# Optimization experiments

Measured on AMD Instinct MI355X. Metric: run time of the kernel, lower is better.

The kernel has to match this reference:

```python
import jax, jax.numpy as jnp
import numpy as np
import math

B, N, D = 128, 64, 2
H, M, L = 64, 64, 2
OMEGA = 1.0


def setup_inputs() -> dict:
    key = jax.random.key(0)
    ks = jax.random.split(key, 32)
    s = 0.1  # param scale
    rn = lambda k, shp: jax.random.normal(k, shp, dtype=jnp.float32) * s
    inp = {
        "x": jax.random.normal(ks[0], (B, N, D), dtype=jnp.float32),
        "spin": jnp.zeros((B, N, 1), jnp.float32),
        "node_w1": rn(ks[1], (D + 1, H)), "node_b1": rn(ks[2], (H,)),
        "node_w2": rn(ks[3], (H, H)), "node_b2": rn(ks[4], (H,)),
        "edge_w1": rn(ks[5], (D + 2, M)), "edge_b1": rn(ks[6], (M,)),
        "edge_w2": rn(ks[7], (M, M)), "edge_b2": rn(ks[8], (M,)),
        "v2e_w1": rn(ks[9], (L, H + M, M)), "v2e_b1": rn(ks[10], (L, M)),
        "v2e_w2": rn(ks[11], (L, M, M)), "v2e_b2": rn(ks[12], (L, M)),
        "e2v_w1": rn(ks[13], (L, M, H)), "e2v_b1": rn(ks[14], (L, H)),
        "e2v_w2": rn(ks[15], (L, H, H)), "e2v_b2": rn(ks[16], (L, H)),
        "head_w1": rn(ks[17], (H, H)), "head_b1": rn(ks[18], (H,)),
        "head_w2": rn(ks[19], (H, D)), "head_b2": rn(ks[20], (D,)),
        # bf_scale_init=0.3 -> softplus-inverse
        "scale": jnp.array([math.log(math.exp(0.3) - 1.0)], jnp.float32),
    }
    return inp


def _mlp(x, w1, b1, w2, b2, act):
    return act(x @ w1 + b1) @ w2 + b2


def reference(x, spin, node_w1, node_b1, node_w2, node_b2,
              edge_w1, edge_b1, edge_w2, edge_b2,
              v2e_w1, v2e_b1, v2e_w2, v2e_b2,
              e2v_w1, e2v_b1, e2v_w2, e2v_b2,
              head_w1, head_b1, head_w2, head_b2, scale):
    gelu = lambda t: jax.nn.gelu(t, approximate=False)  # torch exact GELU
    b, n, d = x.shape
    xs = x * jnp.float32(math.sqrt(OMEGA))
    # node embedding: [B,N,H]
    hv = _mlp(jnp.concatenate([xs, spin], -1), node_w1, node_b1, node_w2, node_b2, gelu)
    # dense pairwise edge features; dr[b,i,j] = xs[b,j] - xs[b,i]
    dr = xs[:, None, :, :] - xs[:, :, None, :]            # [B,N,N,D]
    r2 = jnp.sum(dr * dr, axis=-1, keepdims=True)          # [B,N,N,1]
    rr = jnp.sqrt(r2 + 1e-12)
    he = _mlp(jnp.concatenate([dr, rr, r2], -1), edge_w1, edge_b1, edge_w2, edge_b2, gelu)  # [B,N,N,M]
    # mask excludes self-edges (i==j) from aggregation (they were never created
    # in the original edge list; their dense entries never influence off-diag values)
    mask = (1.0 - jnp.eye(n, dtype=x.dtype))[None, :, :, None]
    inv = jnp.float32(1.0 / max(n - 1, 1))
    for l in range(v2e_w1.shape[0]):
        hvb = jnp.broadcast_to(hv[:, :, None, :], (b, n, n, hv.shape[-1]))  # source node i
        he = _mlp(jnp.concatenate([hvb, he], -1), v2e_w1[l], v2e_b1[l], v2e_w2[l], v2e_b2[l], gelu)
        m = _mlp(he, e2v_w1[l], e2v_b1[l], e2v_w2[l], e2v_b2[l], gelu)      # [B,N,N,H]
        hv = hv + jnp.sum(m * mask, axis=1) * inv           # scatter-add over sources i into j
    dx = _mlp(hv, head_w1, head_b1, head_w2, head_b2, jnp.tanh) * jax.nn.softplus(scale[0])
    return dx - jnp.mean(dx, axis=1, keepdims=True)
```

## Files before the change

kernel.cpp:

```cpp
#include <hip/hip_runtime.h>
#include <math.h>


typedef unsigned short u16;
typedef unsigned int u32;
typedef _Float16 half8 __attribute__((ext_vector_type(8)));
typedef __attribute__((ext_vector_type(4))) float floatx4;

#define TS 72
#define HROW 72
#define HBLK (64 * HROW)

__device__ __forceinline__ float gelu_f(float x) {
    float s = fabsf(x) * 0.70710678118654752f;
    float q = fmaf(fmaf(fmaf(fmaf(0.078108f, s, 0.000972f), s, 0.230389f), s, 0.278393f), s, 1.0f);
    float q2 = q * q;
    float r = __builtin_amdgcn_rcpf(q2 * q2);
    float t = 0.5f * x * r;
    return x > 0.f ? x - t : t;
}

__global__ __launch_bounds__(256) void k_pre(
    const float* __restrict__ ew2, const float* __restrict__ w1he0,
    const float* __restrict__ w2_0, const float* __restrict__ u1_0,
    const float* __restrict__ w1he1, const float* __restrict__ w2_1,
    const float* __restrict__ u1_1,
    const float* __restrict__ eb2, const float* __restrict__ b2_0,
    const float* __restrict__ c1_0, const float* __restrict__ b2_1,
    const float* __restrict__ c1_1,
    const float* __restrict__ b1_0v, const float* __restrict__ b1nv,
    const float* __restrict__ u2_0, const float* __restrict__ u2_1,
    const float* __restrict__ w1n, const float* __restrict__ hw1,
    _Float16* __restrict__ WF,
    float* __restrict__ biasB, float* __restrict__ biasC, float* __restrict__ biasD,
    float* __restrict__ u2_0T, float* __restrict__ u2_1T,
    float* __restrict__ w1nT, float* __restrict__ hw1T,
    const float* __restrict__ x, const float* __restrict__ spin,
    const float* __restrict__ nw1, const float* __restrict__ nb1,
    const float* __restrict__ nw2, const float* __restrict__ nb2,
    const float* __restrict__ w1_0,
    float* __restrict__ hv, float* __restrict__ p0)
{
    int blk = blockIdx.x;
    if (blk < 64) {
        int s = blk >> 4;
        int idx = (blk & 15) * 256 + threadIdx.x;
        int k = idx >> 6, n = idx & 63;
        const float *A, *Bm;
        if (s == 0)      { A = ew2;  Bm = w1he0; }
        else if (s == 1) { A = w2_0; Bm = u1_0;  }
        else if (s == 2) { A = w2_0; Bm = w1he1; }
        else             { A = w2_1; Bm = u1_1;  }
        float acc = 0.f;
        for (int q = 0; q < 64; ++q) acc = fmaf(A[k * 64 + q], Bm[q * 64 + n], acc);
        int kc = k >> 5, qd = (k >> 3) & 3, jj = k & 7;
        WF[(((s * 2 + kc) * 64 + n) * 4 + qd) * 8 + jj] = (_Float16)acc;
    } else if (blk == 64) {
        int s = threadIdx.x >> 6, cc = threadIdx.x & 63;
        if (s > 0) {
            const float *bv, *Bm, *add; float* dst;
            if (s == 1)      { bv = b2_0; Bm = u1_0;  add = c1_0; dst = biasB; }
            else if (s == 2) { bv = b2_0; Bm = w1he1; add = b1nv; dst = biasC; }
            else             { bv = b2_1; Bm = u1_1;  add = c1_1; dst = biasD; }
            float acc = add[cc];
            for (int q = 0; q < 64; ++q) acc = fmaf(bv[q], Bm[q * 64 + cc], acc);
            dst[cc] = acc;
        }
    } else if (blk < 129) {
        int idx = (blk - 65) * 256 + threadIdx.x;
        int s = idx >> 12, r = idx & 4095, m = r >> 6, tc = r & 63;
        const float* W = s == 0 ? u2_0 : s == 1 ? u2_1 : s == 2 ? w1n : hw1;
        float* WT      = s == 0 ? u2_0T : s == 1 ? u2_1T : s == 2 ? w1nT : hw1T;
        WT[tc * 64 + m] = W[m * 64 + tc];
    } else {
        __shared__ float a[4][64];
        __shared__ float shv[4][64];
        int w = threadIdx.x >> 6, h = threadIdx.x & 63;
        int node = (blk - 129) * 4 + w;
        float2 xv = ((const float2*)x)[node];
        float sp = spin[node];
        float z = fmaf(xv.x, nw1[h], fmaf(xv.y, nw1[64 + h], fmaf(sp, nw1[128 + h], nb1[h])));
        a[w][h] = gelu_f(z);
        float acc = nb2[h];
        for (int k = 0; k < 64; ++k) acc = fmaf(a[w][k], nw2[k * 64 + h], acc);
        hv[node * 64 + h] = acc;
        shv[w][h] = acc;
        float pa = b1_0v[h];
        for (int q = 0; q < 64; ++q) pa = fmaf(eb2[q], w1he0[q * 64 + h], pa);
        for (int k = 0; k < 64; ++k) pa = fmaf(shv[w][k], w1_0[k * 64 + h], pa);
        p0[node * 64 + h] = pa;
    }
}

__device__ __forceinline__ void mfma_acc2(
    const _Float16* __restrict__ tA0, const _Float16* __restrict__ tA1,
    const _Float16* __restrict__ WF,
    int stage, int c, int quad, int nn, floatx4 acc0[4], floatx4 acc1[4])
{
    int sA = ((nn >> 2) & 3) << 3;
    #pragma unroll
    for (int kc = 0; kc < 2; ++kc) {
        half8 bf = *(const half8*)(WF + (((stage * 2 + kc) * 64 + c) * 4 + quad) * 8);
        int k0 = (kc * 32 + quad * 8) ^ sA;
        #pragma unroll
        for (int mt = 0; mt < 4; ++mt) {
            half8 af0 = *(const half8*)(tA0 + (mt * 16 + nn) * TS + k0);
            half8 af1 = *(const half8*)(tA1 + (mt * 16 + nn) * TS + k0);
            acc0[mt] = __builtin_amdgcn_mfma_f32_16x16x32_f16(af0, bf, acc0[mt], 0, 0, 0);
            acc1[mt] = __builtin_amdgcn_mfma_f32_16x16x32_f16(af1, bf, acc1[mt], 0, 0, 0);
        }
    }
}

__device__ __forceinline__ void init_bias(floatx4 acc[4], float bc) {
    #pragma unroll
    for (int mt = 0; mt < 4; ++mt) acc[mt] = (floatx4){bc, bc, bc, bc};
}
__device__ __forceinline__ void init_p(floatx4 acc[4], const float* __restrict__ p,
                                       int rowbase, int c, int quad) {
    #pragma unroll
    for (int mt = 0; mt < 4; ++mt)
        #pragma unroll
        for (int r = 0; r < 4; ++r)
            acc[mt][r] = p[(rowbase + mt * 16 + quad * 4 + r) * 64 + c];
}

__global__ __launch_bounds__(256, 4) void k_L0(
    const float* __restrict__ x,
    const float* __restrict__ ew1, const float* __restrict__ eb1,
    const float* __restrict__ p0,
    const float* __restrict__ biasB,
    const float* __restrict__ u2_0T, const float* __restrict__ c2_0,
    const _Float16* __restrict__ WF,
    const float* __restrict__ hv0, float* __restrict__ hv1,
    const float* __restrict__ w1nT, const float* __restrict__ biasC,
    float* __restrict__ p1,
    u16* __restrict__ he0g)
{
    __shared__ __align__(16) _Float16 tA0[64 * TS];
    __shared__ __align__(16) _Float16 tA1[64 * TS];
    __shared__ float sS0[64], sS1[64];
    __shared__ float shv[2][64];
    __shared__ float sredA[256], sredB[256];
    int t = threadIdx.x, L = t & 63;
    int w = __builtin_amdgcn_readfirstlane(t >> 6);
    int nn = L & 15, quad = L >> 4;
    int c = w * 16 + nn;
    int cw = c ^ (quad << 3);
    int b = blockIdx.x >> 5, jp = blockIdx.x & 31;
    int j0 = jp * 2, j1 = j0 + 1;

    float2 xi = ((const float2*)x)[b * 64 + L];
    float2 xa = ((const float2*)x)[b * 64 + j0];
    float2 xb = ((const float2*)x)[b * 64 + j1];
    float da0 = xa.x - xi.x, da1 = xa.y - xi.y;
    float r2a = fmaf(da0, da0, da1 * da1);
    float rra = sqrtf(r2a + 1e-12f);
    float db0 = xb.x - xi.x, db1 = xb.y - xi.y;
    float r2b = fmaf(db0, db0, db1 * db1);
    float rrb = sqrtf(r2b + 1e-12f);
    int swL = ((L >> 2) & 3) << 3;

    #pragma unroll
    for (int mb = 0; mb < 2; ++mb) {
        int m0 = w * 16 + mb * 8;
        half8 h8a, h8b;
        #pragma unroll
        for (int kk = 0; kk < 8; ++kk) {
            int m = m0 + kk;
            float e0 = ew1[m], e1 = ew1[64 + m], e2 = ew1[128 + m], e3 = ew1[192 + m], e4 = eb1[m];
            float za = fmaf(da0, e0, fmaf(da1, e1, fmaf(rra, e2, fmaf(r2a, e3, e4))));
            float zb = fmaf(db0, e0, fmaf(db1, e1, fmaf(rrb, e2, fmaf(r2b, e3, e4))));
            h8a[kk] = (_Float16)gelu_f(za);
            h8b[kk] = (_Float16)gelu_f(zb);
        }
        *(half8*)(tA0 + L * TS + (m0 ^ swL)) = h8a;
        *(half8*)(tA1 + L * TS + (m0 ^ swL)) = h8b;
    }
    __syncthreads();

    floatx4 acc0[4], acc1[4];
    init_p(acc0, p0, b * 64, c, quad);
    #pragma unroll
    for (int mt = 0; mt < 4; ++mt) acc1[mt] = acc0[mt];
    mfma_acc2(tA0, tA1, WF, 0, c, quad, nn, acc0, acc1);
    __syncthreads();
    {
        u16* dst0 = he0g + (size_t)(b * 64 + j0) * HBLK;
        u16* dst1 = he0g + (size_t)(b * 64 + j1) * HBLK;
        #pragma unroll
        for (int mt = 0; mt < 4; ++mt)
            #pragma unroll
            for (int r = 0; r < 4; ++r) {
                int i = mt * 16 + quad * 4 + r;
                _Float16 ya = (_Float16)gelu_f(acc0[mt][r]);
                _Float16 yb = (_Float16)gelu_f(acc1[mt][r]);
                tA0[i * TS + cw] = ya;
                tA1[i * TS + cw] = yb;
                dst0[i * HROW + cw] = __builtin_bit_cast(u16, ya);
                dst1[i * HROW + cw] = __builtin_bit_cast(u16, yb);
            }
    }
    __syncthreads();
    {
        float bb = biasB[c];
        init_bias(acc0, bb);
        init_bias(acc1, bb);
    }
    mfma_acc2(tA0, tA1, WF, 1, c, quad, nn, acc0, acc1);
    {
        float s0 = 0.f, s1 = 0.f;
        #pragma unroll
        for (int mt = 0; mt < 4; ++mt)
            #pragma unroll
            for (int r = 0; r < 4; ++r) {
                int i = mt * 16 + quad * 4 + r;
                float ga = gelu_f(acc0[mt][r]);
                float gb = gelu_f(acc1[mt][r]);
                s0 += (i == j0) ? 0.f : ga;
                s1 += (i == j1) ? 0.f : gb;
            }
        s0 += __shfl_xor(s0, 16); s0 += __shfl_xor(s0, 32);
        s1 += __shfl_xor(s1, 16); s1 += __shfl_xor(s1, 32);
        if (quad == 0) { sS0[c] = s0; sS1[c] = s1; }
    }
    __syncthreads();
    {
        const float4* sv0 = (const float4*)(sS0 + w * 16);
        const float4* sv1 = (const float4*)(sS1 + w * 16);
        const float4* uv4 = (const float4*)(u2_0T + L * 64 + w * 16);
        float g0 = 0.f, g1 = 0.f;
        #pragma unroll
        for (int m4 = 0; m4 < 4; ++m4) {
            float4 uv = uv4[m4], a0 = sv0[m4], a1 = sv1[m4];
            g0 = fmaf(a0.x, uv.x, fmaf(a0.y, uv.y, fmaf(a0.z, uv.z, fmaf(a0.w, uv.w, g0))));
            g1 = fmaf(a1.x, uv.x, fmaf(a1.y, uv.y, fmaf(a1.z, uv.z, fmaf(a1.w, uv.w, g1))));
        }
        sredA[w * 64 + L] = g0;
        sredB[w * 64 + L] = g1;
    }
    __syncthreads();
    if (t < 128) {
        int h = t & 63, sj = t >> 6;
        const float* sr = sj ? sredB : sredA;
        float g = sr[h] + sr[64 + h] + sr[128 + h] + sr[192 + h];
        int jj = sj ? j1 : j0;
        int o = (b * 64 + jj) * 64 + h;
        float hvv = hv0[o] + g * (1.0f / 63.0f) + c2_0[h];
        hv1[o] = hvv;
        shv[sj][h] = hvv;
    }
    __syncthreads();
    {
        const float4* h0 = (const float4*)(shv[0] + w * 16);
        const float4* h1 = (const float4*)(shv[1] + w * 16);
        const float4* wv4 = (const float4*)(w1nT + L * 64 + w * 16);
        float pa = 0.f, pb = 0.f;
        #pragma unroll
        for (int m4 = 0; m4 < 4; ++m4) {
            float4 wv = wv4[m4], a0 = h0[m4], a1 = h1[m4];
            pa = fmaf(a0.x, wv.x, fmaf(a0.y, wv.y, fmaf(a0.z, wv.z, fmaf(a0.w, wv.w, pa))));
            pb = fmaf(a1.x, wv.x, fmaf(a1.y, wv.y, fmaf(a1.z, wv.z, fmaf(a1.w, wv.w, pb))));
        }
        sredA[w * 64 + L] = pa;
        sredB[w * 64 + L] = pb;
    }
    __syncthreads();
    if (t < 128) {
        int h = t & 63, sj = t >> 6;
        const float* sr = sj ? sredB : sredA;
        int jj = sj ? j1 : j0;
        p1[(b * 64 + jj) * 64 + h] = biasC[h] + sr[h] + sr[64 + h] + sr[128 + h] + sr[192 + h];
    }
}

__global__ __launch_bounds__(256, 4) void k_L1(
    const u16* __restrict__ he0g,
    const float* __restrict__ p1,
    const float* __restrict__ biasD,
    const float* __restrict__ u2_1T, const float* __restrict__ c2_1,
    const _Float16* __restrict__ WF,
    const float* __restrict__ hv1,
    const float* __restrict__ hw1T, const float* __restrict__ hb1,
    const float* __restrict__ hw2, const float* __restrict__ hb2,
    const float* __restrict__ scale, float* __restrict__ dx)
{
    __shared__ __align__(16) _Float16 tA0[64 * TS];
    __shared__ __align__(16) _Float16 tA1[64 * TS];
    __shared__ float sS0[64], sS1[64];
    __shared__ float shv[2][64];
    __shared__ float sredA[256], sredB[256];
    int t = threadIdx.x, L = t & 63;
    int w = __builtin_amdgcn_readfirstlane(t >> 6);
    int nn = L & 15, quad = L >> 4;
    int c = w * 16 + nn;
    int cw = c ^ (quad << 3);
    int b = blockIdx.x >> 5, jp = blockIdx.x & 31;
    int j0 = jp * 2, j1 = j0 + 1;

    {
        const float4* s0 = (const float4*)(he0g + (size_t)(b * 64 + j0) * HBLK);
        const float4* s1 = (const float4*)(he0g + (size_t)(b * 64 + j1) * HBLK);
        float4* d0 = (float4*)tA0;
        float4* d1 = (float4*)tA1;
        for (int q = t; q < (HBLK * 2 / 16); q += 256) { d0[q] = s0[q]; d1[q] = s1[q]; }
    }
    __syncthreads();

    floatx4 acc0[4], acc1[4];
    init_p(acc0, p1, b * 64, c, quad);
    #pragma unroll
    for (int mt = 0; mt < 4; ++mt) acc1[mt] = acc0[mt];
    mfma_acc2(tA0, tA1, WF, 2, c, quad, nn, acc0, acc1);
    __syncthreads();
    #pragma unroll
    for (int mt = 0; mt < 4; ++mt)
        #pragma unroll
        for (int r = 0; r < 4; ++r) {
            int i = mt * 16 + quad * 4 + r;
            tA0[i * TS + cw] = (_Float16)gelu_f(acc0[mt][r]);
            tA1[i * TS + cw] = (_Float16)gelu_f(acc1[mt][r]);
        }
    __syncthreads();
    {
        float bd = biasD[c];
        init_bias(acc0, bd);
        init_bias(acc1, bd);
    }
    mfma_acc2(tA0, tA1, WF, 3, c, quad, nn, acc0, acc1);
    {
        float s0 = 0.f, s1 = 0.f;
        #pragma unroll
        for (int mt = 0; mt < 4; ++mt)
            #pragma unroll
            for (int r = 0; r < 4; ++r) {
                int i = mt * 16 + quad * 4 + r;
                float ga = gelu_f(acc0[mt][r]);
                float gb = gelu_f(acc1[mt][r]);
                s0 += (i == j0) ? 0.f : ga;
                s1 += (i == j1) ? 0.f : gb;
            }
        s0 += __shfl_xor(s0, 16); s0 += __shfl_xor(s0, 32);
        s1 += __shfl_xor(s1, 16); s1 += __shfl_xor(s1, 32);
        if (quad == 0) { sS0[c] = s0; sS1[c] = s1; }
    }
    __syncthreads();
    {
        const float4* sv0 = (const float4*)(sS0 + w * 16);
        const float4* sv1 = (const float4*)(sS1 + w * 16);
        const float4* uv4 = (const float4*)(u2_1T + L * 64 + w * 16);
        float g0 = 0.f, g1 = 0.f;
        #pragma unroll
        for (int m4 = 0; m4 < 4; ++m4) {
            float4 uv = uv4[m4], a0 = sv0[m4], a1 = sv1[m4];
            g0 = fmaf(a0.x, uv.x, fmaf(a0.y, uv.y, fmaf(a0.z, uv.z, fmaf(a0.w, uv.w, g0))));
            g1 = fmaf(a1.x, uv.x, fmaf(a1.y, uv.y, fmaf(a1.z, uv.z, fmaf(a1.w, uv.w, g1))));
        }
        sredA[w * 64 + L] = g0;
        sredB[w * 64 + L] = g1;
    }
    __syncthreads();
    if (t < 128) {
        int h = t & 63, sj = t >> 6;
        const float* sr = sj ? sredB : sredA;
        float g = sr[h] + sr[64 + h] + sr[128 + h] + sr[192 + h];
        int jj = sj ? j1 : j0;
        float hv2 = hv1[(b * 64 + jj) * 64 + h] + g * (1.0f / 63.0f) + c2_1[h];
        shv[sj][h] = hv2;
    }
    __syncthreads();
    {
        const float4* h0 = (const float4*)(shv[0] + w * 16);
        const float4* h1 = (const float4*)(shv[1] + w * 16);
        const float4* wv4 = (const float4*)(hw1T + L * 64 + w * 16);
        float a0 = 0.f, a1 = 0.f;
        #pragma unroll
        for (int m4 = 0; m4 < 4; ++m4) {
            float4 wv = wv4[m4], v0 = h0[m4], v1 = h1[m4];
            a0 = fmaf(v0.x, wv.x, fmaf(v0.y, wv.y, fmaf(v0.z, wv.z, fmaf(v0.w, wv.w, a0))));
            a1 = fmaf(v1.x, wv.x, fmaf(v1.y, wv.y, fmaf(v1.z, wv.z, fmaf(v1.w, wv.w, a1))));
        }
        sredA[w * 64 + L] = a0;
        sredB[w * 64 + L] = a1;
    }
    __syncthreads();
    if (t < 128) {
        int h = t & 63, sj = t >> 6;
        const float* sr = sj ? sredB : sredA;
        float a = hb1[h] + sr[h] + sr[64 + h] + sr[128 + h] + sr[192 + h];
        float t1 = tanhf(a);
        float dd0 = t1 * hw2[h * 2], dd1 = t1 * hw2[h * 2 + 1];
        #pragma unroll
        for (int off = 1; off <= 32; off <<= 1) { dd0 += __shfl_xor(dd0, off); dd1 += __shfl_xor(dd1, off); }
        if (h == 0) {
            int jj = sj ? j1 : j0;
            float sp = log1pf(__expf(scale[0]));
            dx[(b * 64 + jj) * 2 + 0] = (dd0 + hb2[0]) * sp;
            dx[(b * 64 + jj) * 2 + 1] = (dd1 + hb2[1]) * sp;
        }
    }
}

__global__ __launch_bounds__(64) void k_mean(
    const float* __restrict__ dx, float* __restrict__ out)
{
    __shared__ float s0[64], s1[64];
    int b = blockIdx.x, j = threadIdx.x;
    float2 d = ((const float2*)dx)[b * 64 + j];
    s0[j] = d.x; s1[j] = d.y;
    __syncthreads();
    float m0 = 0.f, m1 = 0.f;
    for (int q = 0; q < 64; ++q) { m0 += s0[q]; m1 += s1[q]; }
    ((float2*)out)[b * 64 + j] = make_float2(d.x - m0 * (1.0f / 64.0f), d.y - m1 * (1.0f / 64.0f));
}

__global__ void k_beacon(float* out, float code) { out[0] = code; }

extern "C" void kernel_launch(void* const* d_in, const int* in_sizes, int n_in,
                              void* d_out, int out_size, void* d_ws, size_t ws_size,
                              hipStream_t stream)
{
    static const int exp_sizes[23] = {
        16384, 8192, 192, 64, 4096, 64,
        256, 64, 4096, 64,
        16384, 128, 8192, 128,
        8192, 128, 8192, 128,
        4096, 64, 128, 2, 1
    };
    float* hv0 = (float*)d_ws;
    float* hv1 = hv0 + 524288;
    float* p0  = hv1 + 524288;
    float* p1  = p0  + 524288;
    float* dx  = p1  + 524288;
    float* u2_0T = dx + 16384;
    float* u2_1T = u2_0T + 4096;
    float* w1nT  = u2_1T + 4096;
    float* hw1T  = w1nT + 4096;
    float* biasB = hw1T + 4096;
    float* biasC = biasB + 64;
    float* biasD = biasC + 64;
    _Float16* WF = (_Float16*)(biasD + 64);
    u16* he0g  = (u16*)(WF + 16384);
    const size_t need = (size_t)((char*)(he0g + (size_t)8192 * HBLK) - (char*)d_ws);

    int bad = -1;
    if (n_in != 23 || out_size != 16384) bad = 98;
    else if (ws_size < need) bad = 97;
    else for (int i = 0; i < 23; ++i)
        if (in_sizes[i] != exp_sizes[i]) { bad = i; break; }
    if (bad >= 0) {
        k_beacon<<<1, 1, 0, stream>>>((float*)d_out, 2e6f + bad * 1e4f);
        return;
    }

    const float* x      = (const float*)d_in[0];
    const float* spin   = (const float*)d_in[1];
    const float* nw1    = (const float*)d_in[2];
    const float* nb1    = (const float*)d_in[3];
    const float* nw2    = (const float*)d_in[4];
    const float* nb2    = (const float*)d_in[5];
    const float* ew1    = (const float*)d_in[6];
    const float* eb1    = (const float*)d_in[7];
    const float* ew2    = (const float*)d_in[8];
    const float* eb2    = (const float*)d_in[9];
    const float* v2e_w1 = (const float*)d_in[10];
    const float* v2e_b1 = (const float*)d_in[11];
    const float* v2e_w2 = (const float*)d_in[12];
    const float* v2e_b2 = (const float*)d_in[13];
    const float* e2v_w1 = (const float*)d_in[14];
    const float* e2v_b1 = (const float*)d_in[15];
    const float* e2v_w2 = (const float*)d_in[16];
    const float* e2v_b2 = (const float*)d_in[17];
    const float* hw1    = (const float*)d_in[18];
    const float* hb1    = (const float*)d_in[19];
    const float* hw2    = (const float*)d_in[20];
    const float* hb2    = (const float*)d_in[21];
    const float* scale  = (const float*)d_in[22];

    k_pre<<<2177, 256, 0, stream>>>(
        ew2, v2e_w1 + 4096, v2e_w2, e2v_w1,
        v2e_w1 + 12288, v2e_w2 + 4096, e2v_w1 + 4096,
        eb2, v2e_b2, e2v_b1, v2e_b2 + 64, e2v_b1 + 64,
        v2e_b1, v2e_b1 + 64,
        e2v_w2, e2v_w2 + 4096, v2e_w1 + 8192, hw1,
        WF, biasB, biasC, biasD,
        u2_0T, u2_1T, w1nT, hw1T,
        x, spin, nw1, nb1, nw2, nb2, v2e_w1, hv0, p0);
    k_L0<<<4096, 256, 0, stream>>>(x, ew1, eb1,
        p0, biasB, u2_0T, e2v_b2,
        WF, hv0, hv1,
        w1nT, biasC, p1,
        he0g);
    k_L1<<<4096, 256, 0, stream>>>(he0g,
        p1, biasD, u2_1T, e2v_b2 + 64,
        WF, hv1, hw1T, hb1, hw2, hb2, scale, dx);
    k_mean<<<128, 64, 0, stream>>>(dx, (float*)d_out);
}
```

Measured before the change: 212.1 us.

## Process four target nodes per 512-thread block and coalesce he0 spill through LDS

k_L0 and k_L1 now use 512-thread blocks covering four target nodes, laid out as two groups of four waves in one shared buffer. Each group keeps its two-tile MFMA pipeline. The layer-0 edge features are no longer written to global memory as scattered 16-bit stores from registers. They are staged in LDS and copied out with contiguous float4 stores of the whole four-node region, and k_L1 reads that region back the same way. This is meant to cut uncoalesced global writes and halve the block count, at the cost of more LDS per block, a larger sync scope and a changed occupancy profile.

```diff
diff --git a/kernel.cpp b/kernel.cpp
--- a/kernel.cpp
+++ b/kernel.cpp
@@ -10,6 +10,7 @@
 #define TS 72
 #define HROW 72
 #define HBLK (64 * HROW)
+#define TILEB (64 * TS * 2)
 
 __device__ __forceinline__ float gelu_f(float x) {
     float s = fabsf(x) * 0.70710678118654752f;
@@ -104,10 +105,9 @@
         int k0 = (kc * 32 + quad * 8) ^ sA;
         #pragma unroll
         for (int mt = 0; mt < 4; ++mt) {
-            half8 af0 = *(const half8*)(tA0 + (mt * 16 + nn) * TS + k0);
-            half8 af1 = *(const half8*)(tA1 + (mt * 16 + nn) * TS + k0);
-            acc0[mt] = __builtin_amdgcn_mfma_f32_16x16x32_f16(af0, bf, acc0[mt], 0, 0, 0);
-            acc1[mt] = __builtin_amdgcn_mfma_f32_16x16x32_f16(af1, bf, acc1[mt], 0, 0, 0);
+            int off = (mt * 16 + nn) * TS + k0;
+            acc0[mt] = __builtin_amdgcn_mfma_f32_16x16x32_f16(*(const half8*)(tA0 + off), bf, acc0[mt], 0, 0, 0);
+            acc1[mt] = __builtin_amdgcn_mfma_f32_16x16x32_f16(*(const half8*)(tA1 + off), bf, acc1[mt], 0, 0, 0);
         }
     }
 }
@@ -125,7 +125,7 @@
             acc[mt][r] = p[(rowbase + mt * 16 + quad * 4 + r) * 64 + c];
 }
 
-__global__ __launch_bounds__(256, 4) void k_L0(
+__global__ __launch_bounds__(512, 8) void k_L0(
     const float* __restrict__ x,
     const float* __restrict__ ew1, const float* __restrict__ eb1,
     const float* __restrict__ p0,
@@ -137,45 +137,45 @@
     float* __restrict__ p1,
     u16* __restrict__ he0g)
 {
-    __shared__ __align__(16) _Float16 tA0[64 * TS];
-    __shared__ __align__(16) _Float16 tA1[64 * TS];
-    __shared__ float sS0[64], sS1[64];
-    __shared__ float shv[2][64];
-    __shared__ float sredA[256], sredB[256];
+    __shared__ __align__(16) char smem[4 * TILEB + 1024];
+    float* sS   = (float*)(smem + 4 * TILEB);
+    float* sred = (float*)smem;
+    float* shv  = (float*)(smem + TILEB);
+
     int t = threadIdx.x, L = t & 63;
-    int w = __builtin_amdgcn_readfirstlane(t >> 6);
+    int wl = __builtin_amdgcn_readfirstlane((t >> 6) & 3);
+    int g  = __builtin_amdgcn_readfirstlane(t >> 8);
     int nn = L & 15, quad = L >> 4;
-    int c = w * 16 + nn;
+    int c = wl * 16 + nn;
     int cw = c ^ (quad << 3);
-    int b = blockIdx.x >> 5, jp = blockIdx.x & 31;
-    int j0 = jp * 2, j1 = j0 + 1;
+    int b = blockIdx.x >> 4, jp = blockIdx.x & 15;
+    int ja = jp * 4 + g * 2, jb = ja + 1;
+    _Float16* tX0 = (_Float16*)(smem + (2 * g) * TILEB);
+    _Float16* tX1 = (_Float16*)(smem + (2 * g + 1) * TILEB);
 
     float2 xi = ((const float2*)x)[b * 64 + L];
-    float2 xa = ((const float2*)x)[b * 64 + j0];
-    float2 xb = ((const float2*)x)[b * 64 + j1];
+    float2 xa = ((const float2*)x)[b * 64 + ja];
+    float2 xb = ((const float2*)x)[b * 64 + jb];
     float da0 = xa.x - xi.x, da1 = xa.y - xi.y;
-    float r2a = fmaf(da0, da0, da1 * da1);
-    float rra = sqrtf(r2a + 1e-12f);
+    float r2a = fmaf(da0, da0, da1 * da1), rra = sqrtf(r2a + 1e-12f);
     float db0 = xb.x - xi.x, db1 = xb.y - xi.y;
-    float r2b = fmaf(db0, db0, db1 * db1);
-    float rrb = sqrtf(r2b + 1e-12f);
+    float r2b = fmaf(db0, db0, db1 * db1), rrb = sqrtf(r2b + 1e-12f);
     int swL = ((L >> 2) & 3) << 3;
 
     #pragma unroll
     for (int mb = 0; mb < 2; ++mb) {
-        int m0 = w * 16 + mb * 8;
+        int m0 = wl * 16 + mb * 8;
         half8 h8a, h8b;
         #pragma unroll
         for (int kk = 0; kk < 8; ++kk) {
             int m = m0 + kk;
             float e0 = ew1[m], e1 = ew1[64 + m], e2 = ew1[128 + m], e3 = ew1[192 + m], e4 = eb1[m];
-            float za = fmaf(da0, e0, fmaf(da1, e1, fmaf(rra, e2, fmaf(r2a, e3, e4))));
-            float zb = fmaf(db0, e0, fmaf(db1, e1, fmaf(rrb, e2, fmaf(r2b, e3, e4))));
-            h8a[kk] = (_Float16)gelu_f(za);
-            h8b[kk] = (_Float16)gelu_f(zb);
-        }
-        *(half8*)(tA0 + L * TS + (m0 ^ swL)) = h8a;
-        *(half8*)(tA1 + L * TS + (m0 ^ swL)) = h8b;
+            h8a[kk] = (_Float16)gelu_f(fmaf(da0, e0, fmaf(da1, e1, fmaf(rra, e2, fmaf(r2a, e3, e4)))));
+            h8b[kk] = (_Float16)gelu_f(fmaf(db0, e0, fmaf(db1, e1, fmaf(rrb, e2, fmaf(r2b, e3, e4)))));
+        }
+        int o = L * TS + (m0 ^ swL);
+        *(half8*)(tX0 + o) = h8a;
+        *(half8*)(tX1 + o) = h8b;
     }
     __syncthreads();
 
@@ -183,98 +183,90 @@
     init_p(acc0, p0, b * 64, c, quad);
     #pragma unroll
     for (int mt = 0; mt < 4; ++mt) acc1[mt] = acc0[mt];
-    mfma_acc2(tA0, tA1, WF, 0, c, quad, nn, acc0, acc1);
-    __syncthreads();
-    {
-        u16* dst0 = he0g + (size_t)(b * 64 + j0) * HBLK;
-        u16* dst1 = he0g + (size_t)(b * 64 + j1) * HBLK;
+    mfma_acc2(tX0, tX1, WF, 0, c, quad, nn, acc0, acc1);
+    __syncthreads();
+    #pragma unroll
+    for (int mt = 0; mt < 4; ++mt)
+        #pragma unroll
+        for (int r = 0; r < 4; ++r) {
+            int i = mt * 16 + quad * 4 + r;
+            tX0[i * TS + cw] = (_Float16)gelu_f(acc0[mt][r]);
+            tX1[i * TS + cw] = (_Float16)gelu_f(acc1[mt][r]);
+        }
+    __syncthreads();
+    {
+        float4* dst = (float4*)(he0g + (size_t)(b * 64 + jp * 4) * HBLK);
+        const float4* src = (const float4*)smem;
+        for (int q = t; q < 2304; q += 512) dst[q] = src[q];
+    }
+    {
+        float bb = biasB[c];
+        init_bias(acc0, bb); init_bias(acc1, bb);
+    }
+    mfma_acc2(tX0, tX1, WF, 1, c, quad, nn, acc0, acc1);
+    {
+        float s0 = 0.f, s1 = 0.f;
         #pragma unroll
         for (int mt = 0; mt < 4; ++mt)
             #pragma unroll
             for (int r = 0; r < 4; ++r) {
                 int i = mt * 16 + quad * 4 + r;
-                _Float16 ya = (_Float16)gelu_f(acc0[mt][r]);
-                _Float16 yb = (_Float16)gelu_f(acc1[mt][r]);
-                tA0[i * TS + cw] = ya;
-                tA1[i * TS + cw] = yb;
-                dst0[i * HROW + cw] = __builtin_bit_cast(u16, ya);
-                dst1[i * HROW + cw] = __builtin_bit_cast(u16, yb);
-            }
-    }
-    __syncthreads();
-    {
-        float bb = biasB[c];
-        init_bias(acc0, bb);
-        init_bias(acc1, bb);
-    }
-    mfma_acc2(tA0, tA1, WF, 1, c, quad, nn, acc0, acc1);
-    {
-        float s0 = 0.f, s1 = 0.f;
-        #pragma unroll
-        for (int mt = 0; mt < 4; ++mt)
-            #pragma unroll
-            for (int r = 0; r < 4; ++r) {
-                int i = mt * 16 + quad * 4 + r;
-                float ga = gelu_f(acc0[mt][r]);
-                float gb = gelu_f(acc1[mt][r]);
-                s0 += (i == j0) ? 0.f : ga;
-                s1 += (i == j1) ? 0.f : gb;
+                s0 += (i == ja) ? 0.f : gelu_f(acc0[mt][r]);
+                s1 += (i == jb) ? 0.f : gelu_f(acc1[mt][r]);
             }
         s0 += __shfl_xor(s0, 16); s0 += __shfl_xor(s0, 32);
         s1 += __shfl_xor(s1, 16); s1 += __shfl_xor(s1, 32);
-        if (quad == 0) { sS0[c] = s0; sS1[c] = s1; }
-    }
-    __syncthreads();
-    {
-        const float4* sv0 = (const float4*)(sS0 + w * 16);
-        const float4* sv1 = (const float4*)(sS1 + w * 16);
-        const float4* uv4 = (const float4*)(u2_0T + L * 64 + w * 16);
-        float g0 = 0.f, g1 = 0.f;
+        if (quad == 0) { sS[(2 * g) * 64 + c] = s0; sS[(2 * g + 1) * 64 + c] = s1; }
+    }
+    __syncthreads();
+    {
+        const float4* uv4 = (const float4*)(u2_0T + L * 64 + wl * 16);
+        const float4* sv0 = (const float4*)(sS + (2 * g) * 64 + wl * 16);
+        const float4* sv1 = (const float4*)(sS + (2 * g + 1) * 64 + wl * 16);
+        float g0 = 0.f, g1v = 0.f;
         #pragma unroll
         for (int m4 = 0; m4 < 4; ++m4) {
-            float4 uv = uv4[m4], a0 = sv0[m4], a1 = sv1[m4];
-            g0 = fmaf(a0.x, uv.x, fmaf(a0.y, uv.y, fmaf(a0.z, uv.z, fmaf(a0.w, uv.w, g0))));
-            g1 = fmaf(a1.x, uv.x, fmaf(a1.y, uv.y, fmaf(a1.z, uv.z, fmaf(a1.w, uv.w, g1))));
-        }
-        sredA[w * 64 + L] = g0;
-        sredB[w * 64 + L] = g1;
-    }
-    __syncthreads();
-    if (t < 128) {
+            float4 uv = uv4[m4], v0 = sv0[m4], v1 = sv1[m4];
+            g0  = fmaf(v0.x, uv.x, fmaf(v0.y, uv.y, fmaf(v0.z, uv.z, fmaf(v0.w, uv.w, g0))));
+            g1v = fmaf(v1.x, uv.x, fmaf(v1.y, uv.y, fmaf(v1.z, uv.z, fmaf(v1.w, uv.w, g1v))));
+        }
+        sred[(2 * g) * 256 + wl * 64 + L] = g0;
+        sred[(2 * g + 1) * 256 + wl * 64 + L] = g1v;
+    }
+    __syncthreads();
+    if (t < 256) {
         int h = t & 63, sj = t >> 6;
-        const float* sr = sj ? sredB : sredA;
-        float g = sr[h] + sr[64 + h] + sr[128 + h] + sr[192 + h];
-        int jj = sj ? j1 : j0;
-        int o = (b * 64 + jj) * 64 + h;
-        float hvv = hv0[o] + g * (1.0f / 63.0f) + c2_0[h];
+        const float* sr = sred + sj * 256;
+        float gg = sr[h] + sr[64 + h] + sr[128 + h] + sr[192 + h];
+        int o = (b * 64 + jp * 4 + sj) * 64 + h;
+        float hvv = hv0[o] + gg * (1.0f / 63.0f) + c2_0[h];
         hv1[o] = hvv;
-        shv[sj][h] = hvv;
-    }
-    __syncthreads();
-    {
-        const float4* h0 = (const float4*)(shv[0] + w * 16);
-        const float4* h1 = (const float4*)(shv[1] + w * 16);
-        const float4* wv4 = (const float4*)(w1nT + L * 64 + w * 16);
+        shv[sj * 64 + h] = hvv;
+    }
+    __syncthreads();
+    {
+        const float4* wv4 = (const float4*)(w1nT + L * 64 + wl * 16);
+        const float4* h0 = (const float4*)(shv + (2 * g) * 64 + wl * 16);
+        const float4* h1 = (const float4*)(shv + (2 * g + 1) * 64 + wl * 16);
         float pa = 0.f, pb = 0.f;
         #pragma unroll
         for (int m4 = 0; m4 < 4; ++m4) {
-            float4 wv = wv4[m4], a0 = h0[m4], a1 = h1[m4];
-            pa = fmaf(a0.x, wv.x, fmaf(a0.y, wv.y, fmaf(a0.z, wv.z, fmaf(a0.w, wv.w, pa))));
-            pb = fmaf(a1.x, wv.x, fmaf(a1.y, wv.y, fmaf(a1.z, wv.z, fmaf(a1.w, wv.w, pb))));
-        }
-        sredA[w * 64 + L] = pa;
-        sredB[w * 64 + L] = pb;
-    }
-    __syncthreads();
-    if (t < 128) {
+            float4 wv = wv4[m4], v0 = h0[m4], v1 = h1[m4];
+            pa = fmaf(v0.x, wv.x, fmaf(v0.y, wv.y, fmaf(v0.z, wv.z, fmaf(v0.w, wv.w, pa))));
+            pb = fmaf(v1.x, wv.x, fmaf(v1.y, wv.y, fmaf(v1.z, wv.z, fmaf(v1.w, wv.w, pb))));
+        }
+        sred[(2 * g) * 256 + wl * 64 + L] = pa;
+        sred[(2 * g + 1) * 256 + wl * 64 + L] = pb;
+    }
+    __syncthreads();
+    if (t < 256) {
         int h = t & 63, sj = t >> 6;
-        const float* sr = sj ? sredB : sredA;
-        int jj = sj ? j1 : j0;
-        p1[(b * 64 + jj) * 64 + h] = biasC[h] + sr[h] + sr[64 + h] + sr[128 + h] + sr[192 + h];
-    }
-}
-
-__global__ __launch_bounds__(256, 4) void k_L1(
+        const float* sr = sred + sj * 256;
+        p1[(b * 64 + jp * 4 + sj) * 64 + h] = biasC[h] + sr[h] + sr[64 + h] + sr[128 + h] + sr[192 + h];
+    }
+}
+
+__global__ __launch_bounds__(512, 8) void k_L1(
     const u16* __restrict__ he0g,
     const float* __restrict__ p1,
     const float* __restrict__ biasD,
@@ -285,25 +277,26 @@
     const float* __restrict__ hw2, const float* __restrict__ hb2,
     const float* __restrict__ scale, float* __restrict__ dx)
 {
-    __shared__ __align__(16) _Float16 tA0[64 * TS];
-    __shared__ __align__(16) _Float16 tA1[64 * TS];
-    __shared__ float sS0[64], sS1[64];
-    __shared__ float shv[2][64];
-    __shared__ float sredA[256], sredB[256];
+    __shared__ __align__(16) char smem[4 * TILEB + 1024];
+    float* sS   = (float*)(smem + 4 * TILEB);
+    float* sred = (float*)smem;
+    float* shv  = (float*)(smem + TILEB);
+
     int t = threadIdx.x, L = t & 63;
-    int w = __builtin_amdgcn_readfirstlane(t >> 6);
+    int wl = __builtin_amdgcn_readfirstlane((t >> 6) & 3);
+    int g  = __builtin_amdgcn_readfirstlane(t >> 8);
     int nn = L & 15, quad = L >> 4;
-    int c = w * 16 + nn;
+    int c = wl * 16 + nn;
     int cw = c ^ (quad << 3);
-    int b = blockIdx.x >> 5, jp = blockIdx.x & 31;
-    int j0 = jp * 2, j1 = j0 + 1;
-
-    {
-        const float4* s0 = (const float4*)(he0g + (size_t)(b * 64 + j0) * HBLK);
-        const float4* s1 = (const float4*)(he0g + (size_t)(b * 64 + j1) * HBLK);
-        float4* d0 = (float4*)tA0;
-        float4* d1 = (float4*)tA1;
-        for (int q = t; q < (HBLK * 2 / 16); q += 256) { d0[q] = s0[q]; d1[q] = s1[q]; }
+    int b = blockIdx.x >> 4, jp = blockIdx.x & 15;
+    int ja = jp * 4 + g * 2, jb = ja + 1;
+    _Float16* tX0 = (_Float16*)(smem + (2 * g) * TILEB);
+    _Float16* tX1 = (_Float16*)(smem + (2 * g + 1) * TILEB);
+
+    {
+        const float4* src = (const float4*)(he0g + (size_t)(b * 64 + jp * 4) * HBLK);
+        float4* dst = (float4*)smem;
+        for (int q = t; q < 2304; q += 512) dst[q] = src[q];
     }
     __syncthreads();
 
@@ -311,23 +304,22 @@
     init_p(acc0, p1, b * 64, c, quad);
     #pragma unroll
     for (int mt = 0; mt < 4; ++mt) acc1[mt] = acc0[mt];
-    mfma_acc2(tA0, tA1, WF, 2, c, quad, nn, acc0, acc1);
+    mfma_acc2(tX0, tX1, WF, 2, c, quad, nn, acc0, acc1);
     __syncthreads();
     #pragma unroll
     for (int mt = 0; mt < 4; ++mt)
         #pragma unroll
         for (int r = 0; r < 4; ++r) {
             int i = mt * 16 + quad * 4 + r;
-            tA0[i * TS + cw] = (_Float16)gelu_f(acc0[mt][r]);
-            tA1[i * TS + cw] = (_Float16)gelu_f(acc1[mt][r]);
+            tX0[i * TS + cw] = (_Float16)gelu_f(acc0[mt][r]);
+            tX1[i * TS + cw] = (_Float16)gelu_f(acc1[mt][r]);
         }
     __syncthreads();
     {
         float bd = biasD[c];
-        init_bias(acc0, bd);
-        init_bias(acc1, bd);
-    }
-    mfma_acc2(tA0, tA1, WF, 3, c, quad, nn, acc0, acc1);
+        init_bias(acc0, bd); init_bias(acc1, bd);
+    }
+    mfma_acc2(tX0, tX1, WF, 3, c, quad, nn, acc0, acc1);
     {
         float s0 = 0.f, s1 = 0.f;
         #pragma unroll
@@ -335,44 +327,41 @@
             #pragma unroll
             for (int r = 0; r < 4; ++r) {
                 int i = mt * 16 + quad * 4 + r;
-                float ga = gelu_f(acc0[mt][r]);
-                float gb = gelu_f(acc1[mt][r]);
-                s0 += (i == j0) ? 0.f : ga;
-                s1 += (i == j1) ? 0.f : gb;
+                s0 += (i == ja) ? 0.f : gelu_f(acc0[mt][r]);
+                s1 += (i == jb) ? 0.f : gelu_f(acc1[mt][r]);
             }
         s0 += __shfl_xor(s0, 16); s0 += __shfl_xor(s0, 32);
         s1 += __shfl_xor(s1, 16); s1 += __shfl_xor(s1, 32);
-        if (quad == 0) { sS0[c] = s0; sS1[c] = s1; }
-    }
-    __syncthreads();
-    {
-        const float4* sv0 = (const float4*)(sS0 + w * 16);
-        const float4* sv1 = (const float4*)(sS1 + w * 16);
-        const float4* uv4 = (const float4*)(u2_1T + L * 64 + w * 16);
-        float g0 = 0.f, g1 = 0.f;
+        if (quad == 0) { sS[(2 * g) * 64 + c] = s0; sS[(2 * g + 1) * 64 + c] = s1; }
+    }
+    __syncthreads();
+    {
+        const float4* uv4 = (const float4*)(u2_1T + L * 64 + wl * 16);
+        const float4* sv0 = (const float4*)(sS + (2 * g) * 64 + wl * 16);
+        const float4* sv1 = (const float4*)(sS + (2 * g + 1) * 64 + wl * 16);
+        float g0 = 0.f, g1v = 0.f;
         #pragma unroll
         for (int m4 = 0; m4 < 4; ++m4) {
-            float4 uv = uv4[m4], a0 = sv0[m4], a1 = sv1[m4];
-            g0 = fmaf(a0.x, uv.x, fmaf(a0.y, uv.y, fmaf(a0.z, uv.z, fmaf(a0.w, uv.w, g0))));
-            g1 = fmaf(a1.x, uv.x, fmaf(a1.y, uv.y, fmaf(a1.z, uv.z, fmaf(a1.w, uv.w, g1))));
-        }
-        sredA[w * 64 + L] = g0;
-        sredB[w * 64 + L] = g1;
-    }
-    __syncthreads();
-    if (t < 128) {
+            float4 uv = uv4[m4], v0 = sv0[m4], v1 = sv1[m4];
+            g0  = fmaf(v0.x, uv.x, fmaf(v0.y, uv.y, fmaf(v0.z, uv.z, fmaf(v0.w, uv.w, g0))));
+            g1v = fmaf(v1.x, uv.x, fmaf(v1.y, uv.y, fmaf(v1.z, uv.z, fmaf(v1.w, uv.w, g1v))));
+        }
+        sred[(2 * g) * 256 + wl * 64 + L] = g0;
+        sred[(2 * g + 1) * 256 + wl * 64 + L] = g1v;
+    }
+    __syncthreads();
+    if (t < 256) {
         int h = t & 63, sj = t >> 6;
-        const float* sr = sj ? sredB : sredA;
-        float g = sr[h] + sr[64 + h] + sr[128 + h] + sr[192 + h];
-        int jj = sj ? j1 : j0;
-        float hv2 = hv1[(b * 64 + jj) * 64 + h] + g * (1.0f / 63.0f) + c2_1[h];
-        shv[sj][h] = hv2;
-    }
-    __syncthreads();
-    {
-        const float4* h0 = (const float4*)(shv[0] + w * 16);
-        const float4* h1 = (const float4*)(shv[1] + w * 16);
-        const float4* wv4 = (const float4*)(hw1T + L * 64 + w * 16);
+        const float* sr = sred + sj * 256;
+        float gg = sr[h] + sr[64 + h] + sr[128 + h] + sr[192 + h];
+        float hv2 = hv1[(b * 64 + jp * 4 + sj) * 64 + h] + gg * (1.0f / 63.0f) + c2_1[h];
+        shv[sj * 64 + h] = hv2;
+    }
+    __syncthreads();
+    {
+        const float4* wv4 = (const float4*)(hw1T + L * 64 + wl * 16);
+        const float4* h0 = (const float4*)(shv + (2 * g) * 64 + wl * 16);
+        const float4* h1 = (const float4*)(shv + (2 * g + 1) * 64 + wl * 16);
         float a0 = 0.f, a1 = 0.f;
         #pragma unroll
         for (int m4 = 0; m4 < 4; ++m4) {
@@ -380,23 +369,22 @@
             a0 = fmaf(v0.x, wv.x, fmaf(v0.y, wv.y, fmaf(v0.z, wv.z, fmaf(v0.w, wv.w, a0))));
             a1 = fmaf(v1.x, wv.x, fmaf(v1.y, wv.y, fmaf(v1.z, wv.z, fmaf(v1.w, wv.w, a1))));
         }
-        sredA[w * 64 + L] = a0;
-        sredB[w * 64 + L] = a1;
-    }
-    __syncthreads();
-    if (t < 128) {
+        sred[(2 * g) * 256 + wl * 64 + L] = a0;
+        sred[(2 * g + 1) * 256 + wl * 64 + L] = a1;
+    }
+    __syncthreads();
+    if (t < 256) {
         int h = t & 63, sj = t >> 6;
-        const float* sr = sj ? sredB : sredA;
+        const float* sr = sred + sj * 256;
         float a = hb1[h] + sr[h] + sr[64 + h] + sr[128 + h] + sr[192 + h];
         float t1 = tanhf(a);
         float dd0 = t1 * hw2[h * 2], dd1 = t1 * hw2[h * 2 + 1];
         #pragma unroll
         for (int off = 1; off <= 32; off <<= 1) { dd0 += __shfl_xor(dd0, off); dd1 += __shfl_xor(dd1, off); }
         if (h == 0) {
-            int jj = sj ? j1 : j0;
             float sp = log1pf(__expf(scale[0]));
-            dx[(b * 64 + jj) * 2 + 0] = (dd0 + hb2[0]) * sp;
-            dx[(b * 64 + jj) * 2 + 1] = (dd1 + hb2[1]) * sp;
+            dx[(b * 64 + jp * 4 + sj) * 2 + 0] = (dd0 + hb2[0]) * sp;
+            dx[(b * 64 + jp * 4 + sj) * 2 + 1] = (dd1 + hb2[1]) * sp;
         }
     }
 }
@@ -486,12 +474,12 @@
         WF, biasB, biasC, biasD,
         u2_0T, u2_1T, w1nT, hw1T,
         x, spin, nw1, nb1, nw2, nb2, v2e_w1, hv0, p0);
-    k_L0<<<4096, 256, 0, stream>>>(x, ew1, eb1,
+    k_L0<<<2048, 512, 0, stream>>>(x, ew1, eb1,
         p0, biasB, u2_0T, e2v_b2,
         WF, hv0, hv1,
         w1nT, biasC, p1,
         he0g);
-    k_L1<<<4096, 256, 0, stream>>>(he0g,
+    k_L1<<<2048, 512, 0, stream>>>(he0g,
         p1, biasD, u2_1T, e2v_b2 + 64,
         WF, hv1, hw1T, hb1, hw2, hb2, scale, dx);
     k_mean<<<128, 64, 0, stream>>>(dx, (float*)d_out);
```

Result: no change. 210.6 us (-0.7%).
